# Kernel tuning notes

Hardware: AMD Instinct MI355X
Metric: run time of the kernel (lower is better)

Reference implementation:

```python
import jax, jax.numpy as jnp
import numpy as np

D_MODEL = 512
N_HEADS = 8
HEAD_DIM = D_MODEL // N_HEADS
SEQ = 2048
BATCH = 2
EPS = 1e-5
SCALE = 1.0 / np.sqrt(HEAD_DIM).astype(np.float32)
# (kind, window, dilation) per head, matching init_kwargs head_specs
SPECS = [("global", 0, 1), ("global", 0, 1),
         ("window", 64, 1), ("window", 128, 1), ("window", 256, 1),
         ("dilated", 64, 2), ("dilated", 64, 4), ("dilated", 64, 8)]


def build_masks(N):
    i = jnp.arange(N)
    D = jnp.abs(i[:, None] - i[None, :])
    ms = []
    for kind, w, dil in SPECS:
        if kind == "global":
            ms.append(jnp.ones((N, N), dtype=bool))
        elif kind == "window":
            ms.append(D <= w)
        else:  # dilated
            ms.append((D % dil == 0) & (D // dil <= w))
    return jnp.stack(ms)  # [H, N, N] bool


def layernorm(x, g, b):
    mu = jnp.mean(x, axis=-1, keepdims=True)
    var = jnp.mean((x - mu) ** 2, axis=-1, keepdims=True)
    return (x - mu) * jax.lax.rsqrt(var + EPS) * g + b


def setup_inputs() -> dict:
    key = jax.random.key(0)
    ks = jax.random.split(key, 7)
    w = 0.02
    return {
        "x": jax.random.normal(ks[0], (BATCH, SEQ, D_MODEL), dtype=jnp.float32),
        "Wq": jax.random.normal(ks[1], (D_MODEL, D_MODEL), dtype=jnp.float32) * w,
        "Wk": jax.random.normal(ks[2], (D_MODEL, D_MODEL), dtype=jnp.float32) * w,
        "Wv": jax.random.normal(ks[3], (D_MODEL, D_MODEL), dtype=jnp.float32) * w,
        "Wo": jax.random.normal(ks[4], (D_MODEL, D_MODEL), dtype=jnp.float32) * w,
        "T_w1": jax.random.normal(ks[5], (D_MODEL, D_MODEL), dtype=jnp.float32) * w,
        "T_b1": jnp.zeros((D_MODEL,), dtype=jnp.float32),
        "T_w2": jax.random.normal(ks[6], (1, D_MODEL), dtype=jnp.float32) * w,
        "T_b2": jnp.zeros((1,), dtype=jnp.float32),
        "ln_in_g": jnp.ones((D_MODEL,), dtype=jnp.float32),
        "ln_in_b": jnp.zeros((D_MODEL,), dtype=jnp.float32),
        "ln_out_g": jnp.ones((D_MODEL,), dtype=jnp.float32),
        "ln_out_b": jnp.zeros((D_MODEL,), dtype=jnp.float32),
    }


def reference(x, Wq, Wk, Wv, Wo, T_w1, T_b1, T_w2, T_b2,
              ln_in_g, ln_in_b, ln_out_g, ln_out_b):
    B, N, H = x.shape
    x0 = x
    xn = layernorm(x, ln_in_g, ln_in_b)
    # torch Linear: y = x @ W.T ; reshape to [B, h, N, d]
    def heads(W):
        return (xn @ W.T).reshape(B, N, N_HEADS, HEAD_DIM).transpose(0, 2, 1, 3)
    Q, K, V = heads(Wq), heads(Wk), heads(Wv)
    attn = jnp.einsum("bhqd,bhkd->bhqk", Q, K) * SCALE
    mask = build_masks(N)  # [h, N, N]
    attn = jnp.where(mask[None], attn, -jnp.inf)
    attn = jax.nn.softmax(attn, axis=-1)  # every row has diagonal unmasked
    out = jnp.einsum("bhqk,bhkd->bhqd", attn, V)
    out = out.transpose(0, 2, 1, 3).reshape(B, N, N_HEADS * HEAD_DIM)
    out = out @ Wo.T
    # tanh-gated softmax over sequence dim
    T_logits = jnp.tanh(xn @ T_w1.T + T_b1) @ T_w2.T + T_b2  # [B, N, 1]
    T = jax.nn.softmax(T_logits, axis=1)
    out = out * T
    return layernorm(out + x0, ln_out_g, ln_out_b)
```

## Files before the change

kernel.cpp:

```cpp
#include <hip/hip_runtime.h>
#include <math.h>

#define N_SEQ 2048
#define DM    512
#define NTOK  4096
#define NH    8
#define HD    64
#define NSLOT 18

typedef __attribute__((ext_vector_type(8))) short short8;
typedef __attribute__((ext_vector_type(4))) short short4_t;
typedef __attribute__((ext_vector_type(4))) float f32x4;

__device__ inline short f2bf(float x) {
    union { float f; unsigned u; } v; v.f = x;
    unsigned r = v.u + 0x7fff + ((v.u >> 16) & 1);
    return (short)(r >> 16);
}
__device__ inline float bf2f(short s) {
    union { unsigned u; float f; } v; v.u = ((unsigned)(unsigned short)s) << 16;
    return v.f;
}
__device__ inline unsigned pkbf(float a, float b) {
    return ((unsigned)(unsigned short)f2bf(b) << 16) | (unsigned)(unsigned short)f2bf(a);
}
__device__ inline float ftanh(float x) {
    float e = __expf(2.f * x);
    return 1.f - 2.f / (e + 1.f);
}

__device__ inline f32x4 mfma16(short8 a, short8 b, f32x4 c) {
    return __builtin_amdgcn_mfma_f32_16x16x32_bf16(a, b, c, 0, 0, 0);
}

__device__ __forceinline__ void async_cp16(const short* g, short* l) {
    __builtin_amdgcn_global_load_lds(
        (const __attribute__((address_space(1))) void*)g,
        (__attribute__((address_space(3))) void*)l, 16, 0, 0);
}

__global__ __launch_bounds__(256) void k_lncvt(
    const float* __restrict__ x, const float* __restrict__ g,
    const float* __restrict__ b, short* __restrict__ y, float* __restrict__ lg,
    const float* __restrict__ Wq, const float* __restrict__ Wk,
    const float* __restrict__ Wv, const float* __restrict__ Tw1,
    const float* __restrict__ Wo,
    short* __restrict__ wcat, short* __restrict__ wo) {
    int blk = blockIdx.x, t = threadIdx.x;
    if (blk < 2048) {
        int sub = t >> 7, tt = t & 127;
        int tk = blk * 2 + sub;
        if (tt == 0) lg[tk] = 0.f;
        float4 xv = ((const float4*)(x + (size_t)tk * DM))[tt];
        float s = xv.x + xv.y + xv.z + xv.w;
        float q = xv.x*xv.x + xv.y*xv.y + xv.z*xv.z + xv.w*xv.w;
        for (int o = 32; o; o >>= 1) { s += __shfl_down(s, o); q += __shfl_down(q, o); }
        __shared__ float ls[4], lq[4];
        if ((t & 63) == 0) { ls[t >> 6] = s; lq[t >> 6] = q; }
        __syncthreads();
        s = ls[sub * 2] + ls[sub * 2 + 1];
        q = lq[sub * 2] + lq[sub * 2 + 1];
        float mu = s * (1.f / DM);
        float var = q * (1.f / DM) - mu * mu;
        float rs = rsqrtf(var + 1e-5f);
        float4 gv = ((const float4*)g)[tt], bv = ((const float4*)b)[tt];
        short4_t o;
        o[0] = f2bf((xv.x - mu) * rs * gv.x + bv.x);
        o[1] = f2bf((xv.y - mu) * rs * gv.y + bv.y);
        o[2] = f2bf((xv.z - mu) * rs * gv.z + bv.z);
        o[3] = f2bf((xv.w - mu) * rs * gv.w + bv.w);
        *(short4_t*)&y[(size_t)tk * DM + tt * 4] = o;
    } else {
        int id = (blk - 2048) * 256 + t;
        if (id < 262144) {
            int z = id >> 16; int off = id & 65535;
            const float* s = (z == 0) ? Wq : (z == 1) ? Wk : (z == 2) ? Wv : Tw1;
            float4 v = ((const float4*)s)[off];
            short4_t o = {f2bf(v.x), f2bf(v.y), f2bf(v.z), f2bf(v.w)};
            *(short4_t*)(wcat + (size_t)z * 262144 + (size_t)off * 4) = o;
        } else {
            int off = id - 262144;
            float4 v = ((const float4*)Wo)[off];
            short4_t o = {f2bf(v.x), f2bf(v.y), f2bf(v.z), f2bf(v.w)};
            *(short4_t*)(wo + (size_t)off * 4) = o;
        }
    }
}

__global__ __launch_bounds__(256) void k_gemmqkvt(
    const short* __restrict__ A, const short* __restrict__ W,
    const float* __restrict__ Tb1, const float* __restrict__ Tw2,
    short* __restrict__ qb, short* __restrict__ kb, short* __restrict__ vtb,
    float* __restrict__ lg) {
    __shared__ short smem[32768];
    int t = threadIdx.x;
    int lane = t & 63, w = t >> 6;
    int wy = w >> 1, wx = w & 1;
    int ln = lane & 15, q4 = lane >> 4;
    int c0 = blockIdx.x * 128, m0 = blockIdx.y * 128;
    f32x4 acc[4][4];
    f32x4 zero = {0.f, 0.f, 0.f, 0.f};
    #pragma unroll
    for (int i = 0; i < 4; i++)
        #pragma unroll
        for (int j = 0; j < 4; j++) acc[i][j] = zero;
    #pragma unroll
    for (int i2 = 0; i2 < 4; i2++) {
        int id = t + 256 * i2;
        int row = id >> 3, cc = id & 7;
        int scol = (cc ^ (row & 7)) << 3;
        async_cp16(&A[(size_t)(m0 + row) * DM + scol], &smem[id * 8]);
        async_cp16(&W[(size_t)(c0 + row) * DM + scol], &smem[8192 + id * 8]);
    }
    __syncthreads();
    for (int kk = 0; kk < 8; kk++) {
        short* AsB = &smem[(kk & 1) * 16384];
        short* BsB = AsB + 8192;
        if (kk < 7) {
            short* AsN = &smem[((kk & 1) ^ 1) * 16384];
            short* BsN = AsN + 8192;
            int k0 = (kk + 1) * 64;
            #pragma unroll
            for (int i2 = 0; i2 < 4; i2++) {
                int id = t + 256 * i2;
                int row = id >> 3, cc = id & 7;
                int scol = k0 + ((cc ^ (row & 7)) << 3);
                async_cp16(&A[(size_t)(m0 + row) * DM + scol], &AsN[id * 8]);
                async_cp16(&W[(size_t)(c0 + row) * DM + scol], &BsN[id * 8]);
            }
        }
        short8 af[2][4], bfr[2][4];
        #pragma unroll
        for (int ks = 0; ks < 2; ks++) {
            int chnk = ((ks * 4 + q4) ^ (ln & 7)) << 3;
            #pragma unroll
            for (int i = 0; i < 4; i++)
                af[ks][i] = *(short8*)&AsB[(wy * 64 + i * 16 + ln) * 64 + chnk];
            #pragma unroll
            for (int j = 0; j < 4; j++)
                bfr[ks][j] = *(short8*)&BsB[(wx * 64 + j * 16 + ln) * 64 + chnk];
        }
        #pragma unroll
        for (int ks = 0; ks < 2; ks++)
            #pragma unroll
            for (int i = 0; i < 4; i++)
                #pragma unroll
                for (int j = 0; j < 4; j++)
                    acc[i][j] = mfma16(af[ks][i], bfr[ks][j], acc[i][j]);
        __syncthreads();
    }
    short* Es = smem;
    int z = c0 >> 9;
    int bi = m0 >> 11, n0 = m0 & (N_SEQ - 1);
    int hp = (c0 & 511) >> 6;
    if (z < 2) {
        short* dst0 = (z == 0) ? qb : kb;
        float sc2 = (z == 0) ? 0.125f : 1.0f;
        #pragma unroll
        for (int i = 0; i < 4; i++)
            #pragma unroll
            for (int j = 0; j < 4; j++)
                #pragma unroll
                for (int r = 0; r < 4; r++) {
                    int nl = wy * 64 + i * 16 + q4 * 4 + r;
                    int cl = wx * 64 + j * 16 + ln;
                    Es[nl * 136 + cl] = f2bf(acc[i][j][r] * sc2);
                }
        __syncthreads();
        #pragma unroll
        for (int ii = 0; ii < 8; ii++) {
            int id = t + 256 * ii;
            int nl = id >> 4, c8 = id & 15;
            short8 v = *(short8*)&Es[nl * 136 + c8 * 8];
            int hh = hp + (c8 >> 3), d8 = (c8 & 7) * 8;
            *(short8*)&dst0[(((size_t)bi * NH + hh) * N_SEQ + n0 + nl) * HD + d8] = v;
        }
    } else if (z == 2) {
        #pragma unroll
        for (int i = 0; i < 4; i++)
            #pragma unroll
            for (int j = 0; j < 4; j++) {
                int nl0 = wy * 64 + i * 16 + q4 * 4;
                int dl = wx * 64 + j * 16 + ln;
                *(unsigned*)&Es[dl * 136 + nl0]     = pkbf(acc[i][j][0], acc[i][j][1]);
                *(unsigned*)&Es[dl * 136 + nl0 + 2] = pkbf(acc[i][j][2], acc[i][j][3]);
            }
        __syncthreads();
        #pragma unroll
        for (int ii = 0; ii < 8; ii++) {
            int id = t + 256 * ii;
            int dl = id >> 4, nc = id & 15;
            short8 v = *(short8*)&Es[dl * 136 + nc * 8];
            int h = hp + (dl >> 6), d = dl & 63;
            *(short8*)&vtb[(((size_t)bi * NH + h) * HD + d) * N_SEQ + n0 + nc * 8] = v;
        }
    } else {
        #pragma unroll
        for (int i = 0; i < 4; i++) {
            #pragma unroll
            for (int r = 0; r < 4; r++) {
                float s = 0.f;
                #pragma unroll
                for (int j = 0; j < 4; j++) {
                    int tc = (c0 & 511) + wx * 64 + j * 16 + ln;
                    s += ftanh(acc[i][j][r] + Tb1[tc]) * Tw2[tc];
                }
                s += __shfl_xor(s, 1);
                s += __shfl_xor(s, 2);
                s += __shfl_xor(s, 4);
                s += __shfl_xor(s, 8);
                if (ln == 0) {
                    int row = m0 + wy * 64 + i * 16 + q4 * 4 + r;
                    atomicAdd(&lg[row], s);
                }
            }
        }
    }
}

__global__ __launch_bounds__(256) void k_gemmp(
    const short* __restrict__ A, const short* __restrict__ W,
    short* __restrict__ projb) {
    __shared__ short smem[24576];
    int t = threadIdx.x;
    int lane = t & 63, w = t >> 6;
    int wy = w >> 1, wx = w & 1;
    int ln = lane & 15, q4 = lane >> 4;
    int c0 = blockIdx.x * 64, m0 = blockIdx.y * 128;
    f32x4 acc[4][2];
    f32x4 zero = {0.f, 0.f, 0.f, 0.f};
    #pragma unroll
    for (int i = 0; i < 4; i++) { acc[i][0] = zero; acc[i][1] = zero; }
    #pragma unroll
    for (int i2 = 0; i2 < 4; i2++) {
        int id = t + 256 * i2;
        int row = id >> 3, cc = id & 7;
        int scol = (cc ^ (row & 7)) << 3;
        async_cp16(&A[(size_t)(m0 + row) * DM + scol], &smem[id * 8]);
        if (i2 < 2)
            async_cp16(&W[(size_t)(c0 + row) * DM + scol], &smem[8192 + id * 8]);
    }
    __syncthreads();
    for (int kk = 0; kk < 8; kk++) {
        short* AsB = &smem[(kk & 1) * 12288];
        short* BsB = AsB + 8192;
        if (kk < 7) {
            short* AsN = &smem[((kk & 1) ^ 1) * 12288];
            short* BsN = AsN + 8192;
            int k0 = (kk + 1) * 64;
            #pragma unroll
            for (int i2 = 0; i2 < 4; i2++) {
                int id = t + 256 * i2;
                int row = id >> 3, cc = id & 7;
                int scol = k0 + ((cc ^ (row & 7)) << 3);
                async_cp16(&A[(size_t)(m0 + row) * DM + scol], &AsN[id * 8]);
                if (i2 < 2)
                    async_cp16(&W[(size_t)(c0 + row) * DM + scol], &BsN[id * 8]);
            }
        }
        short8 af[2][4], bfr[2][2];
        #pragma unroll
        for (int ks = 0; ks < 2; ks++) {
            int chnk = ((ks * 4 + q4) ^ (ln & 7)) << 3;
            #pragma unroll
            for (int i = 0; i < 4; i++)
                af[ks][i] = *(short8*)&AsB[(wy * 64 + i * 16 + ln) * 64 + chnk];
            #pragma unroll
            for (int j = 0; j < 2; j++)
                bfr[ks][j] = *(short8*)&BsB[(wx * 32 + j * 16 + ln) * 64 + chnk];
        }
        #pragma unroll
        for (int ks = 0; ks < 2; ks++)
            #pragma unroll
            for (int i = 0; i < 4; i++)
                #pragma unroll
                for (int j = 0; j < 2; j++)
                    acc[i][j] = mfma16(af[ks][i], bfr[ks][j], acc[i][j]);
        __syncthreads();
    }
    short* Es = smem;
    #pragma unroll
    for (int i = 0; i < 4; i++)
        #pragma unroll
        for (int j = 0; j < 2; j++)
            #pragma unroll
            for (int r = 0; r < 4; r++) {
                int nl = wy * 64 + i * 16 + q4 * 4 + r;
                int cl = wx * 32 + j * 16 + ln;
                Es[nl * 72 + cl] = f2bf(acc[i][j][r]);
            }
    __syncthreads();
    #pragma unroll
    for (int ii = 0; ii < 4; ii++) {
        int id = t + 256 * ii;
        int nl = id >> 3, c8 = id & 7;
        short8 v = *(short8*)&Es[nl * 72 + c8 * 8];
        *(short8*)&projb[(size_t)(m0 + nl) * DM + c0 + c8 * 8] = v;
    }
}

__global__ __launch_bounds__(256) void k_attn(const short* __restrict__ qb,
                                              const short* __restrict__ kb,
                                              const short* __restrict__ vtb,
                                              short* __restrict__ P_O,
                                              float* __restrict__ P_ml,
                                              short* __restrict__ ob,
                                              const float* __restrict__ lg,
                                              float* __restrict__ gate) {
    __shared__ short Ks[128 * 64];
    __shared__ short Vt[64 * 128];
    __shared__ short Pa[4][16 * 136];
    __shared__ float rg[8];
    int t = threadIdx.x;
    int lane = t & 63, w = t >> 6;
    int ln = lane & 15, q4 = lane >> 4;
    int slot = blockIdx.x, qt = blockIdx.y, bi = blockIdx.z;
    int q0 = qt * 64;
    int h, c;
    if (slot < 4)        { h = 0; c = slot; }
    else if (slot < 8)   { h = 1; c = slot - 4; }
    else if (slot == 8)  { h = 2; c = 0; }
    else if (slot == 9)  { h = 3; c = 0; }
    else if (slot < 12)  { h = 4; c = slot - 10; }
    else if (slot == 12) { h = 5; c = 0; }
    else if (slot < 15)  { h = 6; c = slot - 13; }
    else                 { h = 7; c = slot - 15; }
    int solo = (slot == 8) | (slot == 9) | (slot == 12);
    int kind = (h < 2) ? 0 : (h < 5) ? 1 : 2;
    int wnd = (h == 2 || h >= 5) ? 64 : (h == 3) ? 128 : (h == 4) ? 256 : 0;
    int dsh = (h == 5) ? 1 : (h == 6) ? 2 : (h == 7) ? 3 : 0;
    int dmask = (1 << dsh) - 1;
    int wmax = (kind == 0) ? 0 : (wnd << dsh);
    int tLoU, tHiU, CS;
    if (kind == 0) { tLoU = 0; tHiU = 15; CS = 4; }
    else { tLoU = (q0 - wmax) >> 7; tHiU = (q0 + 63 + wmax) >> 7; CS = 3; }
    int ktLo = tLoU + c * CS;
    int ktHi = ktLo + CS - 1;
    if (ktHi > tHiU) ktHi = tHiU;
    if (ktHi > 15) ktHi = 15;
    if (ktLo < 0) ktLo = 0;
    int p4 = (bi * 32 + qt) * NSLOT + slot;
    float* ml = P_ml + (size_t)p4 * 128;
    if (ktLo > ktHi) {
        if (t < 64) { ml[t] = -1e30f; ml[64 + t] = 0.f; }
        return;
    }
    const size_t base = ((size_t)bi * NH + h) * N_SEQ * HD;
    const short* Q = qb + base;
    const short* K = kb + base;
    const short* Vg = vtb + base;
    short8 qa[2];
    {
        const short* qrow = Q + (size_t)(q0 + w * 16 + ln) * HD + q4 * 8;
        qa[0] = *(const short8*)qrow;
        qa[1] = *(const short8*)(qrow + 32);
    }
    int qi = q0 + w * 16 + ln;
    float m_i = -1e30f, l_i = 0.f;
    f32x4 OT[4];
    f32x4 zero = {0.f, 0.f, 0.f, 0.f};
    #pragma unroll
    for (int d = 0; d < 4; d++) OT[d] = zero;
    short* Paw = Pa[w];
    for (int kt = ktLo; kt <= ktHi; kt++) {
        int k0 = kt << 7;
        __syncthreads();
        #pragma unroll
        for (int i2 = 0; i2 < 4; i2++) {
            int id = t + 256 * i2;
            int kr = id >> 3, ck = id & 7;
            async_cp16(&K[(size_t)(k0 + kr) * HD + ((ck ^ (kr & 7)) << 3)],
                       &Ks[id << 3]);
            int dr = id >> 4, cv = id & 15;
            async_cp16(&Vg[(size_t)dr * N_SEQ + k0 + ((cv ^ (dr & 15)) << 3)],
                       &Vt[id << 3]);
        }
        __syncthreads();
        f32x4 ST[8];
        #pragma unroll
        for (int nt = 0; nt < 8; nt++) ST[nt] = zero;
        __builtin_amdgcn_s_setprio(1);
        #pragma unroll
        for (int nt = 0; nt < 8; nt++) {
            #pragma unroll
            for (int ks = 0; ks < 2; ks++) {
                int cc = ((ks * 4 + q4) ^ (ln & 7)) << 3;
                short8 af = *(short8*)&Ks[(nt * 16 + ln) * 64 + cc];
                ST[nt] = mfma16(af, qa[ks], ST[nt]);
            }
        }
        __builtin_amdgcn_s_setprio(0);
        if (kind != 0) {
            #pragma unroll
            for (int nt = 0; nt < 8; nt++)
                #pragma unroll
                for (int r = 0; r < 4; r++) {
                    int key = k0 + nt * 16 + q4 * 4 + r;
                    int dlt = qi - key; dlt = (dlt < 0) ? -dlt : dlt;
                    int valid;
                    if (kind == 1) valid = (dlt <= wnd);
                    else valid = ((dlt & dmask) == 0) && ((dlt >> dsh) <= wnd);
                    if (!valid) ST[nt][r] = -1e30f;
                }
        }
        float rm = -1e30f;
        #pragma unroll
        for (int nt = 0; nt < 8; nt++) {
            float a = fmaxf(ST[nt][0], ST[nt][1]);
            float b = fmaxf(ST[nt][2], ST[nt][3]);
            rm = fmaxf(rm, fmaxf(a, b));
        }
        rm = fmaxf(rm, __shfl_xor(rm, 16));
        rm = fmaxf(rm, __shfl_xor(rm, 32));
        float mn = fmaxf(m_i, rm);
        float sc = __expf(m_i - mn);
        float rs = 0.f;
        #pragma unroll
        for (int nt = 0; nt < 8; nt++) {
            float p0 = __expf(ST[nt][0] - mn);
            float p1 = __expf(ST[nt][1] - mn);
            float p2 = __expf(ST[nt][2] - mn);
            float p3 = __expf(ST[nt][3] - mn);
            rs += (p0 + p1) + (p2 + p3);
            *(unsigned*)&Paw[ln * 136 + nt * 16 + q4 * 4]     = pkbf(p0, p1);
            *(unsigned*)&Paw[ln * 136 + nt * 16 + q4 * 4 + 2] = pkbf(p2, p3);
        }
        rs += __shfl_xor(rs, 16);
        rs += __shfl_xor(rs, 32);
        l_i = l_i * sc + rs;
        m_i = mn;
        #pragma unroll
        for (int d = 0; d < 4; d++) OT[d] *= sc;
        short8 pb[4];
        #pragma unroll
        for (int ks = 0; ks < 4; ks++)
            pb[ks] = *(short8*)&Paw[ln * 136 + ks * 32 + q4 * 8];
        __builtin_amdgcn_s_setprio(1);
        #pragma unroll
        for (int dt = 0; dt < 4; dt++) {
            #pragma unroll
            for (int ks = 0; ks < 4; ks++) {
                int cc = ((ks * 4 + q4) ^ ln) << 3;
                short8 a = *(short8*)&Vt[(dt * 16 + ln) * 128 + cc];
                OT[dt] = mfma16(a, pb[ks], OT[dt]);
            }
        }
        __builtin_amdgcn_s_setprio(0);
    }
    if (solo) {
        float inv = 1.f / l_i;
        #pragma unroll
        for (int dt = 0; dt < 4; dt++) {
            *(unsigned*)&Paw[ln * 136 + dt * 16 + q4 * 4]     = pkbf(OT[dt][0] * inv, OT[dt][1] * inv);
            *(unsigned*)&Paw[ln * 136 + dt * 16 + q4 * 4 + 2] = pkbf(OT[dt][2] * inv, OT[dt][3] * inv);
        }
        short8 o0 = *(short8*)&Paw[ln * 136 + q4 * 16];
        short8 o1 = *(short8*)&Paw[ln * 136 + q4 * 16 + 8];
        short* dst = ob + ((size_t)bi * N_SEQ + q0 + w * 16 + ln) * DM + h * 64 + q4 * 16;
        *(short8*)dst = o0;
        *(short8*)(dst + 8) = o1;
    } else {
        if (q4 == 0) { ml[w * 16 + ln] = m_i; ml[64 + w * 16 + ln] = l_i; }
        #pragma unroll
        for (int dt = 0; dt < 4; dt++) {
            *(unsigned*)&Paw[ln * 136 + dt * 16 + q4 * 4]     = pkbf(OT[dt][0], OT[dt][1]);
            *(unsigned*)&Paw[ln * 136 + dt * 16 + q4 * 4 + 2] = pkbf(OT[dt][2], OT[dt][3]);
        }
        short8 o0 = *(short8*)&Paw[ln * 136 + q4 * 16];
        short8 o1 = *(short8*)&Paw[ln * 136 + q4 * 16 + 8];
        short* Op = P_O + (size_t)p4 * 4096;
        *(short8*)&Op[(w * 16 + ln) * 64 + q4 * 16] = o0;
        *(short8*)&Op[(w * 16 + ln) * 64 + q4 * 16 + 8] = o1;
    }
    if (slot == 8 && qt == 0) {
        int b = bi;
        float v[8];
        float4 a0 = *(const float4*)&lg[b * N_SEQ + t * 8];
        float4 a1 = *(const float4*)&lg[b * N_SEQ + t * 8 + 4];
        v[0] = a0.x; v[1] = a0.y; v[2] = a0.z; v[3] = a0.w;
        v[4] = a1.x; v[5] = a1.y; v[6] = a1.z; v[7] = a1.w;
        float m = v[0];
        #pragma unroll
        for (int j = 1; j < 8; j++) m = fmaxf(m, v[j]);
        for (int o = 32; o; o >>= 1) m = fmaxf(m, __shfl_down(m, o));
        if ((t & 63) == 0) rg[t >> 6] = m;
        __syncthreads();
        m = fmaxf(fmaxf(rg[0], rg[1]), fmaxf(rg[2], rg[3]));
        float e[8], s = 0.f;
        #pragma unroll
        for (int j = 0; j < 8; j++) { e[j] = __expf(v[j] - m); s += e[j]; }
        for (int o = 32; o; o >>= 1) s += __shfl_down(s, o);
        if ((t & 63) == 0) rg[4 + (t >> 6)] = s;
        __syncthreads();
        s = (rg[4] + rg[5]) + (rg[6] + rg[7]);
        float inv = 1.f / s;
        float4 o0 = {e[0] * inv, e[1] * inv, e[2] * inv, e[3] * inv};
        float4 o1 = {e[4] * inv, e[5] * inv, e[6] * inv, e[7] * inv};
        *(float4*)&gate[b * N_SEQ + t * 8] = o0;
        *(float4*)&gate[b * N_SEQ + t * 8 + 4] = o1;
    }
}

__global__ __launch_bounds__(256) void k_combine(const short* __restrict__ P_O,
                                                 const float* __restrict__ P_ml,
                                                 short* __restrict__ ob) {
    const int hsel[5]  = {0, 1, 4, 6, 7};
    const int hbase[5] = {0, 4, 10, 13, 15};
    const int hcnt[5]  = {4, 4, 2, 2, 3};
    int hh = blockIdx.x, qt = blockIdx.y, bi = blockIdx.z;
    int h = hsel[hh];
    int t = threadIdx.x;
    int row = t >> 2, c0 = (t & 3) * 16;
    int pb = (bi * 32 + qt) * NSLOT + hbase[hh];
    int cnt = hcnt[hh];
    float m = -1e30f;
    for (int s = 0; s < cnt; s++)
        m = fmaxf(m, P_ml[(size_t)(pb + s) * 128 + row]);
    float l = 0.f;
    float acc[16];
    #pragma unroll
    for (int j = 0; j < 16; j++) acc[j] = 0.f;
    for (int s = 0; s < cnt; s++) {
        float ms = P_ml[(size_t)(pb + s) * 128 + row];
        float ls = P_ml[(size_t)(pb + s) * 128 + 64 + row];
        if (ls > 0.f) {
            float sc = __expf(ms - m);
            l += ls * sc;
            const short* Op = P_O + (size_t)(pb + s) * 4096 + row * 64 + c0;
            short8 v0 = *(const short8*)Op;
            short8 v1 = *(const short8*)(Op + 8);
            #pragma unroll
            for (int j = 0; j < 8; j++) acc[j]     += bf2f(v0[j]) * sc;
            #pragma unroll
            for (int j = 0; j < 8; j++) acc[8 + j] += bf2f(v1[j]) * sc;
        }
    }
    float inv = 1.f / l;
    int n = qt * 64 + row;
    short8 o0, o1;
    #pragma unroll
    for (int j = 0; j < 8; j++) o0[j] = f2bf(acc[j] * inv);
    #pragma unroll
    for (int j = 0; j < 8; j++) o1[j] = f2bf(acc[8 + j] * inv);
    short* dst = ob + ((size_t)bi * N_SEQ + n) * DM + h * 64 + c0;
    *(short8*)dst = o0;
    *(short8*)(dst + 8) = o1;
}

__global__ __launch_bounds__(128) void k_final(const short* __restrict__ projb,
                                               const float* __restrict__ gate,
                                               const float* __restrict__ x0,
                                               const float* __restrict__ g,
                                               const float* __restrict__ b,
                                               float* __restrict__ out) {
    int tk = blockIdx.x, t = threadIdx.x;
    float gt = gate[tk];
    short4_t pv = *(const short4_t*)&projb[(size_t)tk * DM + t * 4];
    float4 xv = ((const float4*)(x0 + (size_t)tk * DM))[t];
    float4 y;
    y.x = bf2f(pv[0]) * gt + xv.x;
    y.y = bf2f(pv[1]) * gt + xv.y;
    y.z = bf2f(pv[2]) * gt + xv.z;
    y.w = bf2f(pv[3]) * gt + xv.w;
    float s = y.x + y.y + y.z + y.w;
    float q = y.x*y.x + y.y*y.y + y.z*y.z + y.w*y.w;
    for (int o = 32; o; o >>= 1) { s += __shfl_down(s, o); q += __shfl_down(q, o); }
    __shared__ float ls[2], lq[2];
    if ((t & 63) == 0) { ls[t >> 6] = s; lq[t >> 6] = q; }
    __syncthreads();
    s = ls[0] + ls[1]; q = lq[0] + lq[1];
    float mu = s * (1.f / DM);
    float var = q * (1.f / DM) - mu * mu;
    float rs = rsqrtf(var + 1e-5f);
    float4 gv = ((const float4*)g)[t], bv = ((const float4*)b)[t];
    float4 o;
    o.x = (y.x - mu) * rs * gv.x + bv.x;
    o.y = (y.y - mu) * rs * gv.y + bv.y;
    o.z = (y.z - mu) * rs * gv.z + bv.z;
    o.w = (y.w - mu) * rs * gv.w + bv.w;
    ((float4*)(out + (size_t)tk * DM))[t] = o;
}

extern "C" void kernel_launch(void* const* d_in, const int* in_sizes, int n_in,
                              void* d_out, int out_size, void* d_ws, size_t ws_size,
                              hipStream_t stream) {
    (void)in_sizes; (void)n_in; (void)out_size; (void)ws_size;
    const float* x    = (const float*)d_in[0];
    const float* Wq   = (const float*)d_in[1];
    const float* Wk   = (const float*)d_in[2];
    const float* Wv   = (const float*)d_in[3];
    const float* Wo   = (const float*)d_in[4];
    const float* Tw1  = (const float*)d_in[5];
    const float* Tb1  = (const float*)d_in[6];
    const float* Tw2  = (const float*)d_in[7];
    const float* ling = (const float*)d_in[9];
    const float* linb = (const float*)d_in[10];
    const float* logg = (const float*)d_in[11];
    const float* logb = (const float*)d_in[12];
    float* out = (float*)d_out;

    const size_t SZ = (size_t)NTOK * DM;
    const int NPART = 2 * 32 * NSLOT;
    char* p = (char*)d_ws;
    short* xn   = (short*)p; p += SZ * 2;
    short* wcat = (short*)p; p += (size_t)2048 * DM * 2;
    short* wo   = (short*)p; p += (size_t)DM * DM * 2;
    short* qb   = (short*)p; p += SZ * 2;
    short* kb   = (short*)p; p += SZ * 2;
    short* vtb  = (short*)p; p += SZ * 2;
    short* obuf = (short*)p; p += SZ * 2;
    float* lg   = (float*)p; p += (size_t)NTOK * 4;
    float* gate = (float*)p; p += (size_t)NTOK * 4;
    float* P_ml = (float*)p; p += (size_t)NPART * 128 * 4;
    short* projb = (short*)p;
    short* P_O   = (short*)p; p += (size_t)NPART * 4096 * 2;

    k_lncvt<<<3328, 256, 0, stream>>>(x, ling, linb, xn, lg,
                                      Wq, Wk, Wv, Tw1, Wo, wcat, wo);
    k_gemmqkvt<<<dim3(16, 32), 256, 0, stream>>>(xn, wcat, Tb1, Tw2,
                                                 qb, kb, vtb, lg);
    k_attn<<<dim3(NSLOT, 32, 2), 256, 0, stream>>>(qb, kb, vtb, P_O, P_ml,
                                                   obuf, lg, gate);
    k_combine<<<dim3(5, 32, 2), 256, 0, stream>>>(P_O, P_ml, obuf);
    k_gemmp<<<dim3(8, 32), 256, 0, stream>>>(obuf, wo, projb);
    k_final<<<NTOK, 128, 0, stream>>>(projb, gate, x, logg, logb, out);
}
```

Measured before the change: 151.7 us.

## Compact dilated heads into residue-class subsequences to skip masked key tiles

Dilated heads are now processed per residue class (query index mod dilation). Each block gathers only the strided keys and values that belong to one class, so the mask reduces to a plain window and almost all masked tiles are no longer loaded or computed. The QKV GEMM also writes a row-major V copy for these heads, which the attention kernel transposes in shared memory, and the split slots and combine work for heads 5-7 are removed. This costs an extra V write, strided gathers, and additional in-kernel transposes and syncs.

```diff
diff --git a/kernel.cpp b/kernel.cpp
--- a/kernel.cpp
+++ b/kernel.cpp
@@ -6,7 +6,7 @@
 #define NTOK  4096
 #define NH    8
 #define HD    64
-#define NSLOT 18
+#define NSLOT 15
 
 typedef __attribute__((ext_vector_type(8))) short short8;
 typedef __attribute__((ext_vector_type(4))) short short4_t;
@@ -91,7 +91,7 @@
     const short* __restrict__ A, const short* __restrict__ W,
     const float* __restrict__ Tb1, const float* __restrict__ Tw2,
     short* __restrict__ qb, short* __restrict__ kb, short* __restrict__ vtb,
-    float* __restrict__ lg) {
+    short* __restrict__ vb, float* __restrict__ lg) {
     __shared__ short smem[32768];
     int t = threadIdx.x;
     int lane = t & 63, w = t >> 6;
@@ -176,6 +176,31 @@
             *(short8*)&dst0[(((size_t)bi * NH + hh) * N_SEQ + n0 + nl) * HD + d8] = v;
         }
     } else if (z == 2) {
+        if (hp >= 4) {
+            #pragma unroll
+            for (int i = 0; i < 4; i++)
+                #pragma unroll
+                for (int j = 0; j < 4; j++)
+                    #pragma unroll
+                    for (int r = 0; r < 4; r++) {
+                        int nl = wy * 64 + i * 16 + q4 * 4 + r;
+                        int cl = wx * 64 + j * 16 + ln;
+                        Es[nl * 136 + cl] = f2bf(acc[i][j][r]);
+                    }
+            __syncthreads();
+            #pragma unroll
+            for (int ii = 0; ii < 8; ii++) {
+                int id = t + 256 * ii;
+                int nl = id >> 4, c8 = id & 15;
+                int hh = hp + (c8 >> 3);
+                if (hh >= 5) {
+                    short8 v = *(short8*)&Es[nl * 136 + c8 * 8];
+                    int d8 = (c8 & 7) * 8;
+                    *(short8*)&vb[(((size_t)bi * NH + hh) * N_SEQ + n0 + nl) * HD + d8] = v;
+                }
+            }
+            __syncthreads();
+        }
         #pragma unroll
         for (int i = 0; i < 4; i++)
             #pragma unroll
@@ -302,6 +327,7 @@
 __global__ __launch_bounds__(256) void k_attn(const short* __restrict__ qb,
                                               const short* __restrict__ kb,
                                               const short* __restrict__ vtb,
+                                              const short* __restrict__ vb,
                                               short* __restrict__ P_O,
                                               float* __restrict__ P_ml,
                                               short* __restrict__ ob,
@@ -315,30 +341,35 @@
     int lane = t & 63, w = t >> 6;
     int ln = lane & 15, q4 = lane >> 4;
     int slot = blockIdx.x, qt = blockIdx.y, bi = blockIdx.z;
-    int q0 = qt * 64;
     int h, c;
     if (slot < 4)        { h = 0; c = slot; }
     else if (slot < 8)   { h = 1; c = slot - 4; }
     else if (slot == 8)  { h = 2; c = 0; }
     else if (slot == 9)  { h = 3; c = 0; }
     else if (slot < 12)  { h = 4; c = slot - 10; }
-    else if (slot == 12) { h = 5; c = 0; }
-    else if (slot < 15)  { h = 6; c = slot - 13; }
-    else                 { h = 7; c = slot - 15; }
-    int solo = (slot == 8) | (slot == 9) | (slot == 12);
+    else                 { h = slot - 7; c = 0; }
+    int solo = (slot == 8) | (slot == 9) | (slot >= 12);
     int kind = (h < 2) ? 0 : (h < 5) ? 1 : 2;
-    int wnd = (h == 2 || h >= 5) ? 64 : (h == 3) ? 128 : (h == 4) ? 256 : 0;
-    int dsh = (h == 5) ? 1 : (h == 6) ? 2 : (h == 7) ? 3 : 0;
-    int dmask = (1 << dsh) - 1;
-    int wmax = (kind == 0) ? 0 : (wnd << dsh);
-    int tLoU, tHiU, CS;
-    if (kind == 0) { tLoU = 0; tHiU = 15; CS = 4; }
-    else { tLoU = (q0 - wmax) >> 7; tHiU = (q0 + 63 + wmax) >> 7; CS = 3; }
-    int ktLo = tLoU + c * CS;
-    int ktHi = ktLo + CS - 1;
-    if (ktHi > tHiU) ktHi = tHiU;
-    if (ktHi > 15) ktHi = 15;
-    if (ktLo < 0) ktLo = 0;
+    int wnd = (h == 2 || h >= 5) ? 64 : (h == 3) ? 128 : 256;
+    int dsh = (h >= 5) ? (h - 4) : 0;
+    int ktLo, ktHi, q0m, rres = 0;
+    if (kind == 0) {
+        q0m = qt * 64; ktLo = c * 4; ktHi = ktLo + 3;
+    } else if (kind == 1) {
+        q0m = qt * 64;
+        int tLoU = (q0m - wnd) >> 7, tHiU = (q0m + 63 + wnd) >> 7;
+        ktLo = tLoU + c * 3; ktHi = ktLo + 2;
+        if (ktHi > tHiU) ktHi = tHiU;
+        if (ktHi > 15) ktHi = 15;
+        if (ktLo < 0) ktLo = 0;
+    } else {
+        int nct = 32 >> dsh;
+        rres = qt >> (5 - dsh);
+        q0m = (qt & (nct - 1)) * 64;
+        int Lt = 16 >> dsh;
+        ktLo = (q0m - 64) >> 7; if (ktLo < 0) ktLo = 0;
+        ktHi = (q0m + 127) >> 7; if (ktHi > Lt - 1) ktHi = Lt - 1;
+    }
     int p4 = (bi * 32 + qt) * NSLOT + slot;
     float* ml = P_ml + (size_t)p4 * 128;
     if (ktLo > ktHi) {
@@ -349,13 +380,15 @@
     const short* Q = qb + base;
     const short* K = kb + base;
     const short* Vg = vtb + base;
+    const short* Vr = vb + base;
+    int qm = q0m + w * 16 + ln;
+    int qi = (kind == 2) ? (rres + (qm << dsh)) : qm;
     short8 qa[2];
     {
-        const short* qrow = Q + (size_t)(q0 + w * 16 + ln) * HD + q4 * 8;
+        const short* qrow = Q + (size_t)qi * HD + q4 * 8;
         qa[0] = *(const short8*)qrow;
         qa[1] = *(const short8*)(qrow + 32);
     }
-    int qi = q0 + w * 16 + ln;
     float m_i = -1e30f, l_i = 0.f;
     f32x4 OT[4];
     f32x4 zero = {0.f, 0.f, 0.f, 0.f};
@@ -365,15 +398,28 @@
     for (int kt = ktLo; kt <= ktHi; kt++) {
         int k0 = kt << 7;
         __syncthreads();
-        #pragma unroll
-        for (int i2 = 0; i2 < 4; i2++) {
-            int id = t + 256 * i2;
-            int kr = id >> 3, ck = id & 7;
-            async_cp16(&K[(size_t)(k0 + kr) * HD + ((ck ^ (kr & 7)) << 3)],
-                       &Ks[id << 3]);
-            int dr = id >> 4, cv = id & 15;
-            async_cp16(&Vg[(size_t)dr * N_SEQ + k0 + ((cv ^ (dr & 15)) << 3)],
-                       &Vt[id << 3]);
+        if (kind != 2) {
+            #pragma unroll
+            for (int i2 = 0; i2 < 4; i2++) {
+                int id = t + 256 * i2;
+                int kr = id >> 3, ck = id & 7;
+                async_cp16(&K[(size_t)(k0 + kr) * HD + ((ck ^ (kr & 7)) << 3)],
+                           &Ks[id << 3]);
+                int dr = id >> 4, cv = id & 15;
+                async_cp16(&Vg[(size_t)dr * N_SEQ + k0 + ((cv ^ (dr & 15)) << 3)],
+                           &Vt[id << 3]);
+            }
+        } else {
+            #pragma unroll
+            for (int i2 = 0; i2 < 4; i2++) {
+                int id = t + 256 * i2;
+                int kr = id >> 3, ck = id & 7;
+                int kn = rres + ((k0 + kr) << dsh);
+                async_cp16(&K[(size_t)kn * HD + ((ck ^ (kr & 7)) << 3)],
+                           &Ks[id << 3]);
+                async_cp16(&Vr[(size_t)kn * HD + (ck << 3)],
+                           &Vt[id << 3]);
+            }
         }
         __syncthreads();
         f32x4 ST[8];
@@ -396,11 +442,8 @@
                 #pragma unroll
                 for (int r = 0; r < 4; r++) {
                     int key = k0 + nt * 16 + q4 * 4 + r;
-                    int dlt = qi - key; dlt = (dlt < 0) ? -dlt : dlt;
-                    int valid;
-                    if (kind == 1) valid = (dlt <= wnd);
-                    else valid = ((dlt & dmask) == 0) && ((dlt >> dsh) <= wnd);
-                    if (!valid) ST[nt][r] = -1e30f;
+                    int dlt = qm - key; dlt = (dlt < 0) ? -dlt : dlt;
+                    if (dlt > wnd) ST[nt][r] = -1e30f;
                 }
         }
         float rm = -1e30f;
@@ -431,6 +474,24 @@
         m_i = mn;
         #pragma unroll
         for (int d = 0; d < 4; d++) OT[d] *= sc;
+        if (kind == 2) {
+            int dr = t & 63, cb = t >> 6;
+            short8 tv[4];
+            #pragma unroll
+            for (int e = 0; e < 4; e++) {
+                int c8 = cb + e * 4;
+                #pragma unroll
+                for (int j = 0; j < 8; j++)
+                    tv[e][j] = Vt[(c8 * 8 + j) * 64 + dr];
+            }
+            __syncthreads();
+            #pragma unroll
+            for (int e = 0; e < 4; e++) {
+                int c8 = cb + e * 4;
+                *(short8*)&Vt[dr * 128 + ((c8 ^ (dr & 15)) << 3)] = tv[e];
+            }
+            __syncthreads();
+        }
         short8 pb[4];
         #pragma unroll
         for (int ks = 0; ks < 4; ks++)
@@ -456,7 +517,7 @@
         }
         short8 o0 = *(short8*)&Paw[ln * 136 + q4 * 16];
         short8 o1 = *(short8*)&Paw[ln * 136 + q4 * 16 + 8];
-        short* dst = ob + ((size_t)bi * N_SEQ + q0 + w * 16 + ln) * DM + h * 64 + q4 * 16;
+        short* dst = ob + ((size_t)bi * N_SEQ + qi) * DM + h * 64 + q4 * 16;
         *(short8*)dst = o0;
         *(short8*)(dst + 8) = o1;
     } else {
@@ -504,9 +565,9 @@
 __global__ __launch_bounds__(256) void k_combine(const short* __restrict__ P_O,
                                                  const float* __restrict__ P_ml,
                                                  short* __restrict__ ob) {
-    const int hsel[5]  = {0, 1, 4, 6, 7};
-    const int hbase[5] = {0, 4, 10, 13, 15};
-    const int hcnt[5]  = {4, 4, 2, 2, 3};
+    const int hsel[3]  = {0, 1, 4};
+    const int hbase[3] = {0, 4, 10};
+    const int hcnt[3]  = {4, 4, 2};
     int hh = blockIdx.x, qt = blockIdx.y, bi = blockIdx.z;
     int h = hsel[hh];
     int t = threadIdx.x;
@@ -608,6 +669,7 @@
     short* qb   = (short*)p; p += SZ * 2;
     short* kb   = (short*)p; p += SZ * 2;
     short* vtb  = (short*)p; p += SZ * 2;
+    short* vb   = (short*)p; p += SZ * 2;
     short* obuf = (short*)p; p += SZ * 2;
     float* lg   = (float*)p; p += (size_t)NTOK * 4;
     float* gate = (float*)p; p += (size_t)NTOK * 4;
@@ -618,10 +680,10 @@
     k_lncvt<<<3328, 256, 0, stream>>>(x, ling, linb, xn, lg,
                                       Wq, Wk, Wv, Tw1, Wo, wcat, wo);
     k_gemmqkvt<<<dim3(16, 32), 256, 0, stream>>>(xn, wcat, Tb1, Tw2,
-                                                 qb, kb, vtb, lg);
-    k_attn<<<dim3(NSLOT, 32, 2), 256, 0, stream>>>(qb, kb, vtb, P_O, P_ml,
+                                                 qb, kb, vtb, vb, lg);
+    k_attn<<<dim3(NSLOT, 32, 2), 256, 0, stream>>>(qb, kb, vtb, vb, P_O, P_ml,
                                                    obuf, lg, gate);
-    k_combine<<<dim3(5, 32, 2), 256, 0, stream>>>(P_O, P_ml, obuf);
+    k_combine<<<dim3(3, 32, 2), 256, 0, stream>>>(P_O, P_ml, obuf);
     k_gemmp<<<dim3(8, 32), 256, 0, stream>>>(obuf, wo, projb);
     k_final<<<NTOK, 128, 0, stream>>>(projb, gate, x, logg, logb, out);
 }
```

Result: faster. 145.7 us (median of 2 runs) (-3.9%).
